# Optimization experiments

Measured on AMD Instinct MI355X. Metric: run time of the kernel, lower is better.

## Reference

```python
import jax, jax.numpy as jnp
import numpy as np

HIDDEN = 1024
SCALE = float(np.sqrt(HIDDEN))  # canonical sqrt(d) scale factor


def setup_inputs() -> dict:
    key = jax.random.key(0)
    ks = jax.random.split(key, 10)
    B, S, D = 4, 2048, HIDDEN
    bound = 1.0 / np.sqrt(D)  # torch Linear default init range
    inp = {
        "q": jax.random.normal(ks[0], (B, S, D), dtype=jnp.float32),
        "k": jax.random.normal(ks[1], (B, S, D), dtype=jnp.float32),
        "v": jax.random.normal(ks[2], (B, S, D), dtype=jnp.float32),
        "mask": jnp.zeros((B, S, S), dtype=bool),  # unused by original forward
        "Wq": jax.random.uniform(ks[3], (D, D), jnp.float32, -bound, bound),
        "bq": jax.random.uniform(ks[4], (D,), jnp.float32, -bound, bound),
        "Wk": jax.random.uniform(ks[5], (D, D), jnp.float32, -bound, bound),
        "bk": jax.random.uniform(ks[6], (D,), jnp.float32, -bound, bound),
        "Wv": jax.random.uniform(ks[7], (D, D), jnp.float32, -bound, bound),
        "bv": jax.random.uniform(ks[8], (D,), jnp.float32, -bound, bound),
    }
    return inp


def reference(q, k, v, mask, Wq, bq, Wk, bk, Wv, bv):
    # torch Linear: y = x @ W.T + b
    qp = jnp.einsum("bsd,ed->bse", q, Wq) + bq  # [B,S,D]
    kp = jnp.einsum("bsd,ed->bse", k, Wk) + bk
    vp = jnp.einsum("bsd,ed->bse", v, Wv) + bv
    scores = jnp.einsum("bqd,bkd->bqk", qp, kp) / SCALE  # [B,S,S]
    attn = jax.nn.softmax(scores, axis=-1)
    # dropout with p=0 (dropout_p undefined in source) -> identity
    out = jnp.einsum("bqk,bkd->bqd", attn, vp)  # [B,S,D]
    return out
```

## Files before the change

kernel.cpp:

```cpp
#include <hip/hip_runtime.h>

#define S_ 2048
#define D_ 1024
#define MTOT 8192

typedef __attribute__((ext_vector_type(8))) short bf16x8;
typedef __attribute__((ext_vector_type(8))) unsigned short ush8;
typedef __attribute__((ext_vector_type(4))) unsigned short ush4;
typedef __attribute__((ext_vector_type(4))) float f32x4;

__device__ __forceinline__ unsigned short f2bf(float x) {
    unsigned u = __builtin_bit_cast(unsigned, x);
    u += 0x7fffu + ((u >> 16) & 1u);
    return (unsigned short)(u >> 16);
}

__device__ __forceinline__ void async16(const unsigned short* g, unsigned short* l) {
    __builtin_amdgcn_global_load_lds(
        (const __attribute__((address_space(1))) unsigned int*)(g),
        (__attribute__((address_space(3))) unsigned int*)(l),
        16, 0, 0);
}

#define FENCE() asm volatile("" ::: "memory")
#define SBAR()  __builtin_amdgcn_s_barrier()
#define SCHED0() __builtin_amdgcn_sched_barrier(0)

template<int N> __device__ __forceinline__ void waitv();
template<> __device__ __forceinline__ void waitv<0>() { asm volatile("s_waitcnt vmcnt(0)" ::: "memory"); }
template<> __device__ __forceinline__ void waitv<6>() { asm volatile("s_waitcnt vmcnt(6)" ::: "memory"); }
template<> __device__ __forceinline__ void waitv<8>() { asm volatile("s_waitcnt vmcnt(8)" ::: "memory"); }

__device__ __forceinline__ int xcd_remap(int id, int nwg) {
    return (id & 7) * (nwg >> 3) + (id >> 3);
}

__global__ __launch_bounds__(256)
void tobf16_kernel(const float* __restrict__ s0, const float* __restrict__ s1,
                   const float* __restrict__ s2, const float* __restrict__ s3,
                   const float* __restrict__ s4, const float* __restrict__ s5,
                   const float* __restrict__ bq, const float* __restrict__ bk,
                   const float* __restrict__ bv,
                   unsigned short* __restrict__ d0, unsigned short* __restrict__ d1,
                   unsigned short* __restrict__ d2, unsigned short* __restrict__ d3,
                   unsigned short* __restrict__ d4, unsigned short* __restrict__ d5,
                   float* __restrict__ bias_out)
{
    if (blockIdx.y == 6) {
        if (blockIdx.x != 0) return;
        const int t = threadIdx.x;
        for (int i = t; i < 768; i += 256) {
            const int fidx = i * 4;
            const float* src = (fidx < 1024) ? bq : (fidx < 2048) ? bk : bv;
            reinterpret_cast<float4*>(bias_out)[i] =
                reinterpret_cast<const float4*>(src)[(fidx & 1023) >> 2];
        }
        return;
    }
    const float* src; unsigned short* dst; size_t n;
    switch (blockIdx.y) {
        case 0: src = s0; dst = d0; n = (size_t)MTOT * D_; break;
        case 1: src = s1; dst = d1; n = (size_t)MTOT * D_; break;
        case 2: src = s2; dst = d2; n = (size_t)MTOT * D_; break;
        case 3: src = s3; dst = d3; n = (size_t)D_ * D_;   break;
        case 4: src = s4; dst = d4; n = (size_t)D_ * D_;   break;
        default: src = s5; dst = d5; n = (size_t)D_ * D_;  break;
    }
    size_t base = ((size_t)blockIdx.x * 256 + threadIdx.x) * 8;
    if (base >= n) return;
    float4 a = *reinterpret_cast<const float4*>(src + base);
    float4 b = *reinterpret_cast<const float4*>(src + base + 4);
    ush8 h;
    h[0] = f2bf(a.x); h[1] = f2bf(a.y); h[2] = f2bf(a.z); h[3] = f2bf(a.w);
    h[4] = f2bf(b.x); h[5] = f2bf(b.y); h[6] = f2bf(b.z); h[7] = f2bf(b.w);
    *reinterpret_cast<ush8*>(dst + base) = h;
}

template<int EPI, int BM>
__device__ __forceinline__ void gemm_body(
    unsigned short* As, unsigned short* Bs,
    const unsigned short* __restrict__ Ag, int lda,
    const unsigned short* __restrict__ Bg, int ldb,
    const float* __restrict__ bias,
    float* __restrict__ Cf, unsigned short* __restrict__ Cbf,
    int K, float alpha, int ldc, int m0, int n0, size_t coff)
{
    constexpr int WM    = BM / 2;
    constexpr int MI    = WM / 16;
    constexpr int RQ    = MI / 4;
    constexpr int ASLAB = BM / 64;
    constexpr int SC    = ASLAB + 4;
    constexpr int ABUF  = BM * 64;
    constexpr int BBUF  = 256 * 64;

    const int t = threadIdx.x;
    const int w = t >> 6, lane = t & 63;
    const int wr = w >> 2, wc = w & 3;
    const int lr = lane & 15, lk4 = lane >> 4;

    const int crow = t >> 3;
    const int cj = ((lane & 7) ^ ((lane >> 4) & 3) ^ (((lane >> 3) & 1) << 2)) * 8;

    auto stA = [&](int buf, int s, int kt) {
        async16(Ag + (size_t)(m0 + s * 64 + crow) * lda + kt * 64 + cj,
                As + buf * ABUF + s * 4096 + w * 512);
    };
    auto stB = [&](int buf, int s, int kt) {
        async16(Bg + (size_t)(n0 + s * 64 + crow) * ldb + kt * 64 + cj,
                Bs + buf * BBUF + s * 4096 + w * 512);
    };
    auto rdA = [&](int buf, int rr, int kk) -> bf16x8 {
        const int phys = ((kk * 4 + lk4) ^ ((rr >> 1) & 3) ^ ((rr & 1) << 2)) * 8;
        return *reinterpret_cast<const bf16x8*>(As + buf * ABUF + rr * 64 + phys);
    };
    auto rdB = [&](int buf, int rr, int kk) -> bf16x8 {
        const int phys = ((kk * 4 + lk4) ^ ((rr >> 1) & 3) ^ ((rr & 1) << 2)) * 8;
        return *reinterpret_cast<const bf16x8*>(Bs + buf * BBUF + rr * 64 + phys);
    };

    f32x4 acc[MI][4];
    const f32x4 z4 = {0.f, 0.f, 0.f, 0.f};
#pragma unroll
    for (int i = 0; i < MI; i++)
#pragma unroll
        for (int j = 0; j < 4; j++) acc[i][j] = z4;

    const int NT = K >> 6;

#pragma unroll
    for (int s = 0; s < ASLAB; ++s) stA(0, s, 0);
#pragma unroll
    for (int s = 0; s < 4; ++s)     stB(0, s, 0);
#pragma unroll
    for (int s = 0; s < ASLAB; ++s) stA(1, s, 1);
#pragma unroll
    for (int s = 0; s < 4; ++s)     stB(1, s, 1);
    waitv<SC>(); SCHED0(); SBAR(); FENCE();

    for (int kt = 0; kt < NT; ++kt) {
        const int cur = kt & 1;
        const bool pf = (kt + 2 < NT);

        bf16x8 bfr[4][2];
        bf16x8 af[RQ][2];

#pragma unroll
        for (int ni = 0; ni < 4; ++ni)
#pragma unroll
            for (int kk = 0; kk < 2; ++kk)
                bfr[ni][kk] = rdB(cur, wc * 64 + ni * 16 + lr, kk);
#pragma unroll
        for (int rr = 0; rr < RQ; ++rr)
#pragma unroll
            for (int kk = 0; kk < 2; ++kk)
                af[rr][kk] = rdA(cur, wr * WM + rr * 16 + lr, kk);
        FENCE(); SBAR();
        __builtin_amdgcn_s_setprio(1);
#pragma unroll
        for (int rr = 0; rr < RQ; ++rr)
#pragma unroll
            for (int ni = 0; ni < 4; ++ni)
#pragma unroll
                for (int kk = 0; kk < 2; ++kk)
                    acc[rr][ni] = __builtin_amdgcn_mfma_f32_16x16x32_bf16(af[rr][kk], bfr[ni][kk], acc[rr][ni], 0, 0, 0);
        __builtin_amdgcn_s_setprio(0);
        FENCE(); SBAR();

#pragma unroll
        for (int q = 1; q < 4; ++q) {
#pragma unroll
            for (int rr = 0; rr < RQ; ++rr)
#pragma unroll
                for (int kk = 0; kk < 2; ++kk)
                    af[rr][kk] = rdA(cur, wr * WM + (q * RQ + rr) * 16 + lr, kk);
            if (pf) {
                if (q == 1)      { stB(cur, 0, kt + 2); stB(cur, 1, kt + 2); }
                else if (q == 2) { stB(cur, 2, kt + 2); stB(cur, 3, kt + 2); }
                else if (BM == 256) { stA(cur, 0, kt + 2); stA(cur, 2, kt + 2); }
            }
            FENCE(); SBAR();
            __builtin_amdgcn_s_setprio(1);
#pragma unroll
            for (int rr = 0; rr < RQ; ++rr)
#pragma unroll
                for (int ni = 0; ni < 4; ++ni)
#pragma unroll
                    for (int kk = 0; kk < 2; ++kk)
                        acc[q * RQ + rr][ni] = __builtin_amdgcn_mfma_f32_16x16x32_bf16(af[rr][kk], bfr[ni][kk], acc[q * RQ + rr][ni], 0, 0, 0);
            __builtin_amdgcn_s_setprio(0);
            FENCE(); SBAR();
        }

        if (pf) {
            if (BM == 256) { stA(cur, 1, kt + 2); stA(cur, 3, kt + 2); }
            else           { stA(cur, 0, kt + 2); stA(cur, 1, kt + 2); }
            waitv<SC>(); SCHED0(); SBAR(); FENCE();
        } else if (kt + 1 < NT) {
            waitv<0>(); SCHED0(); SBAR(); FENCE();
        }
    }

#pragma unroll
    for (int mi = 0; mi < MI; ++mi) {
        const int mbase = m0 + wr * WM + mi * 16 + lk4 * 4;
#pragma unroll
        for (int ni = 0; ni < 4; ++ni) {
            const int nn = n0 + wc * 64 + ni * 16 + lr;
            if constexpr (EPI == 0) {
#pragma unroll
                for (int r = 0; r < 4; ++r)
                    Cf[coff + (size_t)(mbase + r) * ldc + nn] = alpha * acc[mi][ni][r];
            } else if constexpr (EPI == 1) {
                const float bb = bias[nn];
#pragma unroll
                for (int r = 0; r < 4; ++r)
                    Cbf[(size_t)(mbase + r) * ldc + nn] = f2bf(acc[mi][ni][r] + bb);
            } else {
                const float bb = bias[nn];
                const int nn2 = nn - 2048;
                const int batch = mbase >> 11, ss = mbase & 2047;
                ush4 hv;
#pragma unroll
                for (int r = 0; r < 4; ++r) hv[r] = f2bf(acc[mi][ni][r] + bb);
                *reinterpret_cast<ush4*>(Cbf + ((size_t)(batch << 10) + nn2) * S_ + ss) = hv;
            }
        }
    }
}

__global__ __launch_bounds__(512, 2)
void proj_fused(const unsigned short* __restrict__ qbf, const unsigned short* __restrict__ kbf,
                const unsigned short* __restrict__ vbf, const unsigned short* __restrict__ wstk,
                const float* __restrict__ bias, unsigned short* __restrict__ QP2,
                unsigned short* __restrict__ vT)
{
    __shared__ unsigned short As[2 * 128 * 64];
    __shared__ unsigned short Bs[2 * 256 * 64];
    int id = xcd_remap(blockIdx.x + 64 * blockIdx.y, 768);
    const int bx = id % 64;
    const int by = id / 64;
    const unsigned short* A = (by < 4) ? qbf : (by < 8) ? kbf : vbf;
    if (by < 8)
        gemm_body<1, 128>(As, Bs, A, D_, wstk, D_, bias, nullptr, QP2,
                          D_, 1.f, 2048, bx * 128, by * 256, 0);
    else
        gemm_body<2, 128>(As, Bs, A, D_, wstk, D_, bias, nullptr, vT,
                          D_, 1.f, 0, bx * 128, by * 256, 0);
}

__global__ __launch_bounds__(512, 2)
void qk256(const unsigned short* __restrict__ QP2, float* __restrict__ sc)
{
    __shared__ unsigned short As[2 * 256 * 64];
    __shared__ unsigned short Bs[2 * 256 * 64];
    int id = xcd_remap(blockIdx.x + 8 * (blockIdx.y + 8 * blockIdx.z), 256);
    const int bx = id % 8; id /= 8;
    const int by = id % 8;
    const int bz = id / 8;
    const unsigned short* base = QP2 + (size_t)bz * S_ * 2048;
    gemm_body<0, 256>(As, Bs, base, 2048, base + 1024, 2048,
                      nullptr, sc, nullptr, D_, 0.03125f, S_,
                      bx * 256, by * 256, (size_t)bz * S_ * S_);
}

__global__ __launch_bounds__(512, 2)
void pv128(const unsigned short* __restrict__ P, const unsigned short* __restrict__ vT,
           float* __restrict__ out)
{
    __shared__ unsigned short As[2 * 128 * 64];
    __shared__ unsigned short Bs[2 * 256 * 64];
    int id = xcd_remap(blockIdx.x + 16 * (blockIdx.y + 4 * blockIdx.z), 256);
    const int bx = id % 16; id /= 16;
    const int by = id % 4;
    const int bz = id / 4;
    gemm_body<0, 128>(As, Bs, P + (size_t)bz * S_ * S_, S_,
                      vT + (size_t)bz * D_ * S_, S_,
                      nullptr, out, nullptr, S_, 1.f, D_,
                      bx * 128, by * 256, (size_t)bz * S_ * D_);
}

__global__ __launch_bounds__(256)
void softmax_kernel(const float* __restrict__ s, unsigned short* __restrict__ P)
{
    const size_t row = blockIdx.x;
    const int t = threadIdx.x;
    const float* sp = s + row * 2048 + (size_t)t * 8;
    float4 a = *reinterpret_cast<const float4*>(sp);
    float4 b = *reinterpret_cast<const float4*>(sp + 4);
    float x[8] = {a.x, a.y, a.z, a.w, b.x, b.y, b.z, b.w};

    float m = x[0];
    for (int j = 1; j < 8; j++) m = fmaxf(m, x[j]);
    for (int off = 1; off < 64; off <<= 1) m = fmaxf(m, __shfl_xor(m, off));
    __shared__ float redm[4], reds[4];
    const int w = t >> 6;
    if ((t & 63) == 0) redm[w] = m;
    __syncthreads();
    m = fmaxf(fmaxf(redm[0], redm[1]), fmaxf(redm[2], redm[3]));

    float e[8]; float sum = 0.f;
    for (int j = 0; j < 8; j++) { e[j] = __expf(x[j] - m); sum += e[j]; }
    for (int off = 1; off < 64; off <<= 1) sum += __shfl_xor(sum, off);
    if ((t & 63) == 0) reds[w] = sum;
    __syncthreads();
    sum = reds[0] + reds[1] + reds[2] + reds[3];
    const float inv = 1.0f / sum;

    ush8 h;
    for (int j = 0; j < 8; j++) h[j] = f2bf(e[j] * inv);
    *reinterpret_cast<ush8*>(P + row * 2048 + (size_t)t * 8) = h;
}

extern "C" void kernel_launch(void* const* d_in, const int* in_sizes, int n_in,
                              void* d_out, int out_size, void* d_ws, size_t ws_size,
                              hipStream_t stream)
{
    const float* q  = (const float*)d_in[0];
    const float* k  = (const float*)d_in[1];
    const float* v  = (const float*)d_in[2];
    const float* Wq = (const float*)d_in[4];
    const float* bq = (const float*)d_in[5];
    const float* Wk = (const float*)d_in[6];
    const float* bk = (const float*)d_in[7];
    const float* Wv = (const float*)d_in[8];
    const float* bv = (const float*)d_in[9];
    float* out = (float*)d_out;

    const size_t MB = (size_t)1 << 20;
    if (ws_size < 200 * MB) return;
    char* ws = (char*)d_ws;
    unsigned short* qbf  = (unsigned short*)(ws + 0 * MB);
    unsigned short* kbf  = (unsigned short*)(ws + 16 * MB);
    unsigned short* vbf  = (unsigned short*)(ws + 32 * MB);
    unsigned short* wstk = (unsigned short*)(ws + 48 * MB);
    float*          bst  = (float*)         (ws + 54 * MB);
    unsigned short* QP2  = (unsigned short*)(ws + 56 * MB);
    unsigned short* vT   = (unsigned short*)(ws + 88 * MB);
    float*          sc   = (float*)         (ws + 104 * MB);
    unsigned short* P    = (unsigned short*)(ws + 168 * MB);

    tobf16_kernel<<<dim3(4096, 7), dim3(256), 0, stream>>>(
        q, k, v, Wq, Wk, Wv, bq, bk, bv,
        qbf, kbf, vbf, wstk, wstk + (size_t)D_ * D_, wstk + 2 * (size_t)D_ * D_, bst);

    proj_fused<<<dim3(64, 12), dim3(512), 0, stream>>>(qbf, kbf, vbf, wstk, bst, QP2, vT);

    qk256<<<dim3(8, 8, 4), dim3(512), 0, stream>>>(QP2, sc);

    softmax_kernel<<<dim3(MTOT), dim3(256), 0, stream>>>(sc, P);

    pv128<<<dim3(16, 4, 4), dim3(512), 0, stream>>>(P, vT, out);
}
```

Measured before the change: 221.3 us.

## Use 256x256 tiles everywhere and co-schedule V projection with QK^T GEMM

The GEMM body is fixed to 256x256 tiles and the BM template parameter is removed. Projections and PV now use bigger tiles with more reuse per block. The V projection is moved out of the Q/K projection launch and runs in the same launch as the QK^T scores GEMM, since the two do not depend on each other, so the grid is fuller. The cost is fewer blocks for PV (128) and projection, which may leave CUs idle on a 256-CU part.

```diff
diff --git a/kernel.cpp b/kernel.cpp
--- a/kernel.cpp
+++ b/kernel.cpp
@@ -76,7 +76,7 @@
     *reinterpret_cast<ush8*>(dst + base) = h;
 }
 
-template<int EPI, int BM>
+template<int EPI>
 __device__ __forceinline__ void gemm_body(
     unsigned short* As, unsigned short* Bs,
     const unsigned short* __restrict__ Ag, int lda,
@@ -85,13 +85,9 @@
     float* __restrict__ Cf, unsigned short* __restrict__ Cbf,
     int K, float alpha, int ldc, int m0, int n0, size_t coff)
 {
-    constexpr int WM    = BM / 2;
-    constexpr int MI    = WM / 16;
-    constexpr int RQ    = MI / 4;
-    constexpr int ASLAB = BM / 64;
-    constexpr int SC    = ASLAB + 4;
-    constexpr int ABUF  = BM * 64;
-    constexpr int BBUF  = 256 * 64;
+    constexpr int MI   = 8;
+    constexpr int RQ   = 2;
+    constexpr int BUF  = 256 * 64;
 
     const int t = threadIdx.x;
     const int w = t >> 6, lane = t & 63;
@@ -103,19 +99,19 @@
 
     auto stA = [&](int buf, int s, int kt) {
         async16(Ag + (size_t)(m0 + s * 64 + crow) * lda + kt * 64 + cj,
-                As + buf * ABUF + s * 4096 + w * 512);
+                As + buf * BUF + s * 4096 + w * 512);
     };
     auto stB = [&](int buf, int s, int kt) {
         async16(Bg + (size_t)(n0 + s * 64 + crow) * ldb + kt * 64 + cj,
-                Bs + buf * BBUF + s * 4096 + w * 512);
+                Bs + buf * BUF + s * 4096 + w * 512);
     };
     auto rdA = [&](int buf, int rr, int kk) -> bf16x8 {
         const int phys = ((kk * 4 + lk4) ^ ((rr >> 1) & 3) ^ ((rr & 1) << 2)) * 8;
-        return *reinterpret_cast<const bf16x8*>(As + buf * ABUF + rr * 64 + phys);
+        return *reinterpret_cast<const bf16x8*>(As + buf * BUF + rr * 64 + phys);
     };
     auto rdB = [&](int buf, int rr, int kk) -> bf16x8 {
         const int phys = ((kk * 4 + lk4) ^ ((rr >> 1) & 3) ^ ((rr & 1) << 2)) * 8;
-        return *reinterpret_cast<const bf16x8*>(Bs + buf * BBUF + rr * 64 + phys);
+        return *reinterpret_cast<const bf16x8*>(Bs + buf * BUF + rr * 64 + phys);
     };
 
     f32x4 acc[MI][4];
@@ -128,14 +124,14 @@
     const int NT = K >> 6;
 
 #pragma unroll
-    for (int s = 0; s < ASLAB; ++s) stA(0, s, 0);
-#pragma unroll
-    for (int s = 0; s < 4; ++s)     stB(0, s, 0);
-#pragma unroll
-    for (int s = 0; s < ASLAB; ++s) stA(1, s, 1);
-#pragma unroll
-    for (int s = 0; s < 4; ++s)     stB(1, s, 1);
-    waitv<SC>(); SCHED0(); SBAR(); FENCE();
+    for (int s = 0; s < 4; ++s) stA(0, s, 0);
+#pragma unroll
+    for (int s = 0; s < 4; ++s) stB(0, s, 0);
+#pragma unroll
+    for (int s = 0; s < 4; ++s) stA(1, s, 1);
+#pragma unroll
+    for (int s = 0; s < 4; ++s) stB(1, s, 1);
+    waitv<8>(); SCHED0(); SBAR(); FENCE();
 
     for (int kt = 0; kt < NT; ++kt) {
         const int cur = kt & 1;
@@ -153,7 +149,7 @@
         for (int rr = 0; rr < RQ; ++rr)
 #pragma unroll
             for (int kk = 0; kk < 2; ++kk)
-                af[rr][kk] = rdA(cur, wr * WM + rr * 16 + lr, kk);
+                af[rr][kk] = rdA(cur, wr * 128 + rr * 16 + lr, kk);
         FENCE(); SBAR();
         __builtin_amdgcn_s_setprio(1);
 #pragma unroll
@@ -172,11 +168,11 @@
             for (int rr = 0; rr < RQ; ++rr)
 #pragma unroll
                 for (int kk = 0; kk < 2; ++kk)
-                    af[rr][kk] = rdA(cur, wr * WM + (q * RQ + rr) * 16 + lr, kk);
+                    af[rr][kk] = rdA(cur, wr * 128 + (q * RQ + rr) * 16 + lr, kk);
             if (pf) {
                 if (q == 1)      { stB(cur, 0, kt + 2); stB(cur, 1, kt + 2); }
                 else if (q == 2) { stB(cur, 2, kt + 2); stB(cur, 3, kt + 2); }
-                else if (BM == 256) { stA(cur, 0, kt + 2); stA(cur, 2, kt + 2); }
+                else             { stA(cur, 0, kt + 2); stA(cur, 2, kt + 2); }
             }
             FENCE(); SBAR();
             __builtin_amdgcn_s_setprio(1);
@@ -192,9 +188,8 @@
         }
 
         if (pf) {
-            if (BM == 256) { stA(cur, 1, kt + 2); stA(cur, 3, kt + 2); }
-            else           { stA(cur, 0, kt + 2); stA(cur, 1, kt + 2); }
-            waitv<SC>(); SCHED0(); SBAR(); FENCE();
+            stA(cur, 1, kt + 2); stA(cur, 3, kt + 2);
+            waitv<8>(); SCHED0(); SBAR(); FENCE();
         } else if (kt + 1 < NT) {
             waitv<0>(); SCHED0(); SBAR(); FENCE();
         }
@@ -202,7 +197,7 @@
 
 #pragma unroll
     for (int mi = 0; mi < MI; ++mi) {
-        const int mbase = m0 + wr * WM + mi * 16 + lk4 * 4;
+        const int mbase = m0 + wr * 128 + mi * 16 + lk4 * 4;
 #pragma unroll
         for (int ni = 0; ni < 4; ++ni) {
             const int nn = n0 + wc * 64 + ni * 16 + lr;
@@ -229,54 +224,60 @@
 }
 
 __global__ __launch_bounds__(512, 2)
-void proj_fused(const unsigned short* __restrict__ qbf, const unsigned short* __restrict__ kbf,
-                const unsigned short* __restrict__ vbf, const unsigned short* __restrict__ wstk,
-                const float* __restrict__ bias, unsigned short* __restrict__ QP2,
-                unsigned short* __restrict__ vT)
-{
-    __shared__ unsigned short As[2 * 128 * 64];
-    __shared__ unsigned short Bs[2 * 256 * 64];
-    int id = xcd_remap(blockIdx.x + 64 * blockIdx.y, 768);
-    const int bx = id % 64;
-    const int by = id / 64;
-    const unsigned short* A = (by < 4) ? qbf : (by < 8) ? kbf : vbf;
-    if (by < 8)
-        gemm_body<1, 128>(As, Bs, A, D_, wstk, D_, bias, nullptr, QP2,
-                          D_, 1.f, 2048, bx * 128, by * 256, 0);
-    else
-        gemm_body<2, 128>(As, Bs, A, D_, wstk, D_, bias, nullptr, vT,
-                          D_, 1.f, 0, bx * 128, by * 256, 0);
-}
-
-__global__ __launch_bounds__(512, 2)
-void qk256(const unsigned short* __restrict__ QP2, float* __restrict__ sc)
+void proj_qk(const unsigned short* __restrict__ qbf, const unsigned short* __restrict__ kbf,
+             const unsigned short* __restrict__ wstk, const float* __restrict__ bias,
+             unsigned short* __restrict__ QP2)
 {
     __shared__ unsigned short As[2 * 256 * 64];
     __shared__ unsigned short Bs[2 * 256 * 64];
-    int id = xcd_remap(blockIdx.x + 8 * (blockIdx.y + 8 * blockIdx.z), 256);
+    int id = xcd_remap(blockIdx.x + 32 * blockIdx.y, 256);
+    const int bx = id % 32;
+    const int by = id / 32;
+    const unsigned short* A = (by < 4) ? qbf : kbf;
+    gemm_body<1>(As, Bs, A, D_, wstk, D_, bias, nullptr, QP2,
+                 D_, 1.f, 2048, bx * 256, by * 256, 0);
+}
+
+__global__ __launch_bounds__(512, 2)
+void qk_projv(const unsigned short* __restrict__ QP2, const unsigned short* __restrict__ vbf,
+              const unsigned short* __restrict__ wstk, const float* __restrict__ bias,
+              float* __restrict__ sc, unsigned short* __restrict__ vT)
+{
+    __shared__ unsigned short As[2 * 256 * 64];
+    __shared__ unsigned short Bs[2 * 256 * 64];
+    int id = xcd_remap(blockIdx.x + 128 * blockIdx.y, 384);
+    if (id < 256) {
+        const int bz = id >> 6;
+        const int r  = id & 63;
+        const int bx = r & 7;
+        const int by = r >> 3;
+        const unsigned short* base = QP2 + (size_t)bz * S_ * 2048;
+        gemm_body<0>(As, Bs, base, 2048, base + 1024, 2048,
+                     nullptr, sc, nullptr, D_, 0.03125f, S_,
+                     bx * 256, by * 256, (size_t)bz * S_ * S_);
+    } else {
+        const int idv = id - 256;
+        const int bx = idv & 31;
+        const int by = idv >> 5;
+        gemm_body<2>(As, Bs, vbf, D_, wstk, D_, bias, nullptr, vT,
+                     D_, 1.f, 0, bx * 256, 2048 + by * 256, 0);
+    }
+}
+
+__global__ __launch_bounds__(512, 2)
+void pv256(const unsigned short* __restrict__ P, const unsigned short* __restrict__ vT,
+           float* __restrict__ out)
+{
+    __shared__ unsigned short As[2 * 256 * 64];
+    __shared__ unsigned short Bs[2 * 256 * 64];
+    int id = xcd_remap(blockIdx.x + 8 * (blockIdx.y + 4 * blockIdx.z), 128);
     const int bx = id % 8; id /= 8;
-    const int by = id % 8;
-    const int bz = id / 8;
-    const unsigned short* base = QP2 + (size_t)bz * S_ * 2048;
-    gemm_body<0, 256>(As, Bs, base, 2048, base + 1024, 2048,
-                      nullptr, sc, nullptr, D_, 0.03125f, S_,
-                      bx * 256, by * 256, (size_t)bz * S_ * S_);
-}
-
-__global__ __launch_bounds__(512, 2)
-void pv128(const unsigned short* __restrict__ P, const unsigned short* __restrict__ vT,
-           float* __restrict__ out)
-{
-    __shared__ unsigned short As[2 * 128 * 64];
-    __shared__ unsigned short Bs[2 * 256 * 64];
-    int id = xcd_remap(blockIdx.x + 16 * (blockIdx.y + 4 * blockIdx.z), 256);
-    const int bx = id % 16; id /= 16;
     const int by = id % 4;
     const int bz = id / 4;
-    gemm_body<0, 128>(As, Bs, P + (size_t)bz * S_ * S_, S_,
-                      vT + (size_t)bz * D_ * S_, S_,
-                      nullptr, out, nullptr, S_, 1.f, D_,
-                      bx * 128, by * 256, (size_t)bz * S_ * D_);
+    gemm_body<0>(As, Bs, P + (size_t)bz * S_ * S_, S_,
+                 vT + (size_t)bz * D_ * S_, S_,
+                 nullptr, out, nullptr, S_, 1.f, D_,
+                 bx * 256, by * 256, (size_t)bz * S_ * D_);
 }
 
 __global__ __launch_bounds__(256)
@@ -343,11 +344,11 @@
         q, k, v, Wq, Wk, Wv, bq, bk, bv,
         qbf, kbf, vbf, wstk, wstk + (size_t)D_ * D_, wstk + 2 * (size_t)D_ * D_, bst);
 
-    proj_fused<<<dim3(64, 12), dim3(512), 0, stream>>>(qbf, kbf, vbf, wstk, bst, QP2, vT);
-
-    qk256<<<dim3(8, 8, 4), dim3(512), 0, stream>>>(QP2, sc);
+    proj_qk<<<dim3(32, 8), dim3(512), 0, stream>>>(qbf, kbf, wstk, bst, QP2);
+
+    qk_projv<<<dim3(128, 3), dim3(512), 0, stream>>>(QP2, vbf, wstk, bst, sc, vT);
 
     softmax_kernel<<<dim3(MTOT), dim3(256), 0, stream>>>(sc, P);
 
-    pv128<<<dim3(16, 4, 4), dim3(512), 0, stream>>>(P, vT, out);
-}
+    pv256<<<dim3(8, 4, 4), dim3(512), 0, stream>>>(P, vT, out);
+}
```

New measurement: 236.8 us. 7.0% more time.
